# Kernel tuning notes

Measured on AMD Instinct MI355X. Metric: run time of the kernel, lower is better.

The kernel has to match this reference:

```python
import jax, jax.numpy as jnp
import numpy as np

N_QUBITS = 4
N_LAYERS = 2


def _apply_1q_shared(state, gate, wire):
    # state: [N,2,2,2,2] (axis wire+1 = qubit 'wire'), gate: [2,2] complex
    st = jnp.moveaxis(state, wire + 1, -1)
    st = jnp.einsum('ij,nabcj->nabci', gate, st)
    return jnp.moveaxis(st, -1, wire + 1)


def _apply_1q_batched(state, gate, wire):
    # gate: [N,2,2] (per-sample angles)
    st = jnp.moveaxis(state, wire + 1, -1)
    st = jnp.einsum('nij,nabcj->nabci', gate, st)
    return jnp.moveaxis(st, -1, wire + 1)


def _cnot(state, c, t):
    s0 = jnp.take(state, 0, axis=c + 1)
    s1 = jnp.take(state, 1, axis=c + 1)
    t_ax = t if t > c else t + 1  # target axis after removing control axis
    s1 = jnp.flip(s1, axis=t_ax)
    return jnp.stack([s0, s1], axis=c + 1)


def _ry_mat_batched(theta):
    c = jnp.cos(theta / 2).astype(jnp.complex64)
    s = jnp.sin(theta / 2).astype(jnp.complex64)
    return jnp.stack([jnp.stack([c, -s], -1), jnp.stack([s, c], -1)], -2)


def _rx_mat(theta):
    c = jnp.cos(theta / 2).astype(jnp.complex64)
    s = (-1j * jnp.sin(theta / 2)).astype(jnp.complex64)
    return jnp.array(0).astype(jnp.complex64) + jnp.stack([jnp.stack([c, s]), jnp.stack([s, c])])


def _ry_mat(theta):
    c = jnp.cos(theta / 2).astype(jnp.complex64)
    s = jnp.sin(theta / 2).astype(jnp.complex64)
    return jnp.stack([jnp.stack([c, -s]), jnp.stack([s, c])])


def _rz_mat(theta):
    e = jnp.exp(-0.5j * theta.astype(jnp.complex64))
    z = jnp.zeros((), jnp.complex64)
    return jnp.stack([jnp.stack([e, z]), jnp.stack([z, jnp.conj(e)])])


def setup_inputs() -> dict:
    key = jax.random.key(0)
    k1, k2 = jax.random.split(key)
    x = jax.random.normal(k1, (32, 3, 128, 128), dtype=jnp.float32)
    weights = 0.1 * jax.random.normal(k2, (N_LAYERS, N_QUBITS, 3), dtype=jnp.float32)
    return {'x': x, 'weights': weights}


def reference(x, weights):
    B, C, H, W = x.shape
    # 2x2 patches, stride 1, flattened row-major: [N,4]
    patches = jnp.stack(
        [x[:, :, :-1, :-1], x[:, :, :-1, 1:], x[:, :, 1:, :-1], x[:, :, 1:, 1:]],
        axis=-1,
    ).reshape(-1, 4)
    N = patches.shape[0]

    # |0000> state, axis layout [N, q0, q1, q2, q3] (wire 0 most significant)
    state = jnp.zeros((N, 2, 2, 2, 2), jnp.complex64).at[:, 0, 0, 0, 0].set(1.0)

    # RY data encoding (per-patch angles)
    for q in range(N_QUBITS):
        state = _apply_1q_batched(state, _ry_mat_batched(patches[:, q]), q)

    for layer in range(N_LAYERS):
        for q in range(N_QUBITS):
            state = _apply_1q_shared(state, _rx_mat(weights[layer, q, 0]), q)
            state = _apply_1q_shared(state, _ry_mat(weights[layer, q, 1]), q)
            state = _apply_1q_shared(state, _rz_mat(weights[layer, q, 2]), q)
        state = _cnot(state, 0, 1)
        state = _cnot(state, 2, 3)
        state = _cnot(state, 0, 2)
        state = _cnot(state, 1, 3)

    probs = jnp.abs(state) ** 2  # [N,2,2,2,2] real
    ev = probs[:, 0].sum(axis=(1, 2, 3)) - probs[:, 1].sum(axis=(1, 2, 3))  # <Z0>
    return ev.reshape(B, C, H - 1, W - 1).astype(x.dtype)
```

## Files before the change

### kernel.cpp

```cpp
#include <hip/hip_runtime.h>
#include <hip/hip_bf16.h>


__global__ void qconv_setup(const float* __restrict__ wts, float* __restrict__ W) {
    __shared__ float2 U[16][16];
    __shared__ float  A[16][16];
    const int tid = threadIdx.x;

    if (tid < 16) {
        float2 v[16];
        #pragma unroll
        for (int i = 0; i < 16; ++i) v[i] = make_float2(i == tid ? 1.f : 0.f, 0.f);

        #pragma unroll
        for (int layer = 0; layer < 2; ++layer) {
            #pragma unroll
            for (int q = 0; q < 4; ++q) {
                const int p = 3 - q;
                const float thx = wts[(layer * 4 + q) * 3 + 0];
                const float thy = wts[(layer * 4 + q) * 3 + 1];
                const float thz = wts[(layer * 4 + q) * 3 + 2];
                {
                    float c = __cosf(0.5f * thx), s = __sinf(0.5f * thx);
                    #pragma unroll
                    for (int i = 0; i < 16; ++i) if (!((i >> p) & 1)) {
                        const int j = i | (1 << p);
                        float2 a = v[i], b = v[j];
                        v[i] = make_float2(c * a.x + s * b.y, c * a.y - s * b.x);
                        v[j] = make_float2(c * b.x + s * a.y, c * b.y - s * a.x);
                    }
                }
                {
                    float c = __cosf(0.5f * thy), s = __sinf(0.5f * thy);
                    #pragma unroll
                    for (int i = 0; i < 16; ++i) if (!((i >> p) & 1)) {
                        const int j = i | (1 << p);
                        float2 a = v[i], b = v[j];
                        v[i] = make_float2(c * a.x - s * b.x, c * a.y - s * b.y);
                        v[j] = make_float2(s * a.x + c * b.x, s * a.y + c * b.y);
                    }
                }
                {
                    float c = __cosf(0.5f * thz), s = __sinf(0.5f * thz);
                    #pragma unroll
                    for (int i = 0; i < 16; ++i) {
                        float2 a = v[i];
                        if (!((i >> p) & 1)) v[i] = make_float2(c * a.x + s * a.y, c * a.y - s * a.x);
                        else                 v[i] = make_float2(c * a.x - s * a.y, c * a.y + s * a.x);
                    }
                }
            }
            #pragma unroll
            for (int ee = 0; ee < 4; ++ee) {
                const int cc[4] = {0, 2, 0, 1}, tt[4] = {1, 3, 2, 3};
                const int pc = 3 - cc[ee], pt = 3 - tt[ee];
                #pragma unroll
                for (int i = 0; i < 16; ++i) if (((i >> pc) & 1) && !((i >> pt) & 1)) {
                    const int j = i | (1 << pt);
                    float2 t = v[i]; v[i] = v[j]; v[j] = t;
                }
            }
        }
        #pragma unroll
        for (int i = 0; i < 16; ++i) U[tid][i] = v[i];
    }
    __syncthreads();

    {
        const int j = tid >> 4, k = tid & 15;
        float re = 0.f;
        #pragma unroll
        for (int i = 0; i < 16; ++i) {
            const float z = (i & 8) ? -1.f : 1.f;
            float2 a = U[j][i], b = U[k][i];
            re += z * (a.x * b.x + a.y * b.y);
        }
        A[j][k] = re;
    }
    __syncthreads();

    if (tid < 81) {
        const int e = tid;
        const int d0 = e / 27, d1 = (e / 9) % 3, d2 = (e / 3) % 3, d3 = e % 3;
        int mask1 = 0, mask2 = 0;
        if (d0 == 1) mask1 |= 8; else if (d0 == 2) mask2 |= 8;
        if (d1 == 1) mask1 |= 4; else if (d1 == 2) mask2 |= 4;
        if (d2 == 1) mask1 |= 2; else if (d2 == 2) mask2 |= 2;
        if (d3 == 1) mask1 |= 1; else if (d3 == 2) mask2 |= 1;
        float sum = 0.f;
        #pragma unroll
        for (int b = 0; b < 16; ++b) {
            const float sgn = (__popc(b & mask1) & 1) ? -1.f : 1.f;
            sum += sgn * A[b][b ^ mask2];
        }
        W[e] = sum * 0.0625f;
    }
}

__global__ __launch_bounds__(256) void qconv_main(
        const float* __restrict__ x, const float* __restrict__ Wc,
        float* __restrict__ out, int rows) {
    const int g   = blockIdx.x * blockDim.x + threadIdx.x;
    const int row = g >> 5;
    const int l   = g & 31;
    if (row >= rows) return;

    float w[81];
    {
        const float4* W4 = (const float4*)Wc;
        #pragma unroll
        for (int i = 0; i < 20; ++i) {
            float4 v4 = W4[i];
            w[4*i+0] = v4.x; w[4*i+1] = v4.y; w[4*i+2] = v4.z; w[4*i+3] = v4.w;
        }
        w[80] = Wc[80];
    }

    const int img   = row / 127;
    const int h     = row % 127;
    const int col0  = l * 4;
    const int ncols = (l == 31) ? 3 : 4;
    const int base  = img * 16384 + h * 128 + col0;

    float tp[5], bt[5];
    {
        float4 t4 = *(const float4*)(x + base);
        float4 b4 = *(const float4*)(x + base + 128);
        tp[0] = t4.x; tp[1] = t4.y; tp[2] = t4.z; tp[3] = t4.w;
        bt[0] = b4.x; bt[1] = b4.y; bt[2] = b4.z; bt[3] = b4.w;
        tp[4] = 0.f; bt[4] = 0.f;
        if (ncols == 4) { tp[4] = x[base + 4]; bt[4] = x[base + 132]; }
    }

    float ct[5], st[5], cb[5], sb[5];
    #pragma unroll
    for (int j = 0; j < 5; ++j) {
        __sincosf(tp[j], &st[j], &ct[j]);
        __sincosf(bt[j], &sb[j], &cb[j]);
    }

    float ev[4];
    #pragma unroll
    for (int k = 0; k < 4; ++k) {
        const float c0 = ct[k],     s0 = st[k];
        const float c1 = ct[k + 1], s1 = st[k + 1];
        const float c2 = cb[k],     s2 = sb[k];
        const float c3 = cb[k + 1], s3 = sb[k + 1];
        float acc = 0.f;
        #pragma unroll
        for (int e0 = 0; e0 < 3; ++e0) {
            const float u0 = (e0 == 0) ? 1.f : ((e0 == 1) ? c0 : s0);
            float a0 = 0.f;
            #pragma unroll
            for (int e1 = 0; e1 < 3; ++e1) {
                const float u1 = (e1 == 0) ? 1.f : ((e1 == 1) ? c1 : s1);
                float a1 = 0.f;
                #pragma unroll
                for (int e2 = 0; e2 < 3; ++e2) {
                    const float u2 = (e2 == 0) ? 1.f : ((e2 == 1) ? c2 : s2);
                    const int idx = ((e0 * 3 + e1) * 3 + e2) * 3;
                    const float a2 = w[idx] + w[idx + 1] * c3 + w[idx + 2] * s3;
                    a1 += a2 * u2;
                }
                a0 += a1 * u1;
            }
            acc += a0 * u0;
        }
        ev[k] = acc;
    }

    const int obase = row * 127 + col0;
    #pragma unroll
    for (int k = 0; k < 4; ++k) if (k < ncols) out[obase + k] = ev[k];
}

extern "C" void kernel_launch(void* const* d_in, const int* in_sizes, int n_in,
                              void* d_out, int out_size, void* d_ws, size_t ws_size,
                              hipStream_t stream) {
    const float* x   = (const float*)d_in[0];
    const float* wts = (const float*)d_in[1];
    float* out = (float*)d_out;
    float* W   = (float*)d_ws;

    qconv_setup<<<1, 256, 0, stream>>>(wts, W);

    const int rows    = out_size / 127;
    const int threads = rows * 32;
    const int blocks  = (threads + 255) / 256;
    qconv_main<<<blocks, 256, 0, stream>>>(x, W, out, rows);
}
```

Before: 16.88 us.

## Fuse weight-setup into main kernel and process two output rows per thread

Removes the separate single-block setup kernel: every block now recomputes the 81 collapsed circuit coefficients in shared memory before evaluating patches, eliminating a kernel launch and the global round-trip for W. Each thread also handles two adjacent output rows, loading three input rows and reusing the middle row's sin/cos, which cuts input loads and transcendental work per output. The cost is redundant per-block setup work (a 16x16 unitary build plus reductions in every block) and more live registers, which could lower occupancy.

```diff
diff --git a/kernel.cpp b/kernel.cpp
--- a/kernel.cpp
+++ b/kernel.cpp
@@ -2,7 +2,8 @@
 #include <hip/hip_bf16.h>
 
 
-__global__ void qconv_setup(const float* __restrict__ wts, float* __restrict__ W) {
+__device__ __forceinline__ void compute_W_block(const float* __restrict__ wts,
+                                                float* __restrict__ Wsh) {
     __shared__ float2 U[16][16];
     __shared__ float  A[16][16];
     const int tid = threadIdx.x;
@@ -79,73 +80,81 @@
     }
     __syncthreads();
 
-    if (tid < 81) {
-        const int e = tid;
-        const int d0 = e / 27, d1 = (e / 9) % 3, d2 = (e / 3) % 3, d3 = e % 3;
-        int mask1 = 0, mask2 = 0;
-        if (d0 == 1) mask1 |= 8; else if (d0 == 2) mask2 |= 8;
-        if (d1 == 1) mask1 |= 4; else if (d1 == 2) mask2 |= 4;
-        if (d2 == 1) mask1 |= 2; else if (d2 == 2) mask2 |= 2;
-        if (d3 == 1) mask1 |= 1; else if (d3 == 2) mask2 |= 1;
-        float sum = 0.f;
-        #pragma unroll
-        for (int b = 0; b < 16; ++b) {
-            const float sgn = (__popc(b & mask1) & 1) ? -1.f : 1.f;
-            sum += sgn * A[b][b ^ mask2];
-        }
-        W[e] = sum * 0.0625f;
-    }
+    if (tid < 84) {
+        float r = 0.f;
+        if (tid < 81) {
+            const int e = tid;
+            const int d0 = e / 27, d1 = (e / 9) % 3, d2 = (e / 3) % 3, d3 = e % 3;
+            int mask1 = 0, mask2 = 0;
+            if (d0 == 1) mask1 |= 8; else if (d0 == 2) mask2 |= 8;
+            if (d1 == 1) mask1 |= 4; else if (d1 == 2) mask2 |= 4;
+            if (d2 == 1) mask1 |= 2; else if (d2 == 2) mask2 |= 2;
+            if (d3 == 1) mask1 |= 1; else if (d3 == 2) mask2 |= 1;
+            float sum = 0.f;
+            #pragma unroll
+            for (int b = 0; b < 16; ++b) {
+                const float sgn = (__popc(b & mask1) & 1) ? -1.f : 1.f;
+                sum += sgn * A[b][b ^ mask2];
+            }
+            r = sum * 0.0625f;
+        }
+        Wsh[tid] = r;
+    }
+    __syncthreads();
 }
 
-__global__ __launch_bounds__(256) void qconv_main(
-        const float* __restrict__ x, const float* __restrict__ Wc,
-        float* __restrict__ out, int rows) {
-    const int g   = blockIdx.x * blockDim.x + threadIdx.x;
-    const int row = g >> 5;
-    const int l   = g & 31;
-    if (row >= rows) return;
+__global__ __launch_bounds__(256) void qconv_fused(
+        const float* __restrict__ x, const float* __restrict__ wts,
+        float* __restrict__ out) {
+    __shared__ __align__(16) float Wsh[84];
+    compute_W_block(wts, Wsh);
 
     float w[81];
     {
-        const float4* W4 = (const float4*)Wc;
+        const float4* W4 = (const float4*)Wsh;
         #pragma unroll
         for (int i = 0; i < 20; ++i) {
             float4 v4 = W4[i];
             w[4*i+0] = v4.x; w[4*i+1] = v4.y; w[4*i+2] = v4.z; w[4*i+3] = v4.w;
         }
-        w[80] = Wc[80];
-    }
-
-    const int img   = row / 127;
-    const int h     = row % 127;
-    const int col0  = l * 4;
+        w[80] = Wsh[80];
+    }
+
+    const int g    = blockIdx.x * 8 + (threadIdx.x >> 5);
+    const int l    = threadIdx.x & 31;
+    const int img  = g >> 6;
+    const int pair = g & 63;
+    const int h    = pair * 2;
+    const int nr   = (pair == 63) ? 1 : 2;
+    const int col0 = l * 4;
     const int ncols = (l == 31) ? 3 : 4;
-    const int base  = img * 16384 + h * 128 + col0;
-
-    float tp[5], bt[5];
+    const int base = img * 16384 + h * 128 + col0;
+
+    float r0[5], r1[5], r2[5];
     {
-        float4 t4 = *(const float4*)(x + base);
+        float4 a4 = *(const float4*)(x + base);
         float4 b4 = *(const float4*)(x + base + 128);
-        tp[0] = t4.x; tp[1] = t4.y; tp[2] = t4.z; tp[3] = t4.w;
-        bt[0] = b4.x; bt[1] = b4.y; bt[2] = b4.z; bt[3] = b4.w;
-        tp[4] = 0.f; bt[4] = 0.f;
-        if (ncols == 4) { tp[4] = x[base + 4]; bt[4] = x[base + 132]; }
-    }
-
-    float ct[5], st[5], cb[5], sb[5];
+        r0[0]=a4.x; r0[1]=a4.y; r0[2]=a4.z; r0[3]=a4.w;
+        r1[0]=b4.x; r1[1]=b4.y; r1[2]=b4.z; r1[3]=b4.w;
+        r0[4]=0.f; r1[4]=0.f; r2[0]=0.f; r2[1]=0.f; r2[2]=0.f; r2[3]=0.f; r2[4]=0.f;
+        if (ncols == 4) { r0[4] = x[base + 4]; r1[4] = x[base + 132]; }
+        if (nr == 2) {
+            float4 c4 = *(const float4*)(x + base + 256);
+            r2[0]=c4.x; r2[1]=c4.y; r2[2]=c4.z; r2[3]=c4.w;
+            if (ncols == 4) r2[4] = x[base + 260];
+        }
+    }
+
+    float c0a[5], s0a[5], c1a[5], s1a[5], c2a[5], s2a[5];
     #pragma unroll
     for (int j = 0; j < 5; ++j) {
-        __sincosf(tp[j], &st[j], &ct[j]);
-        __sincosf(bt[j], &sb[j], &cb[j]);
-    }
-
-    float ev[4];
-    #pragma unroll
-    for (int k = 0; k < 4; ++k) {
-        const float c0 = ct[k],     s0 = st[k];
-        const float c1 = ct[k + 1], s1 = st[k + 1];
-        const float c2 = cb[k],     s2 = sb[k];
-        const float c3 = cb[k + 1], s3 = sb[k + 1];
+        __sincosf(r0[j], &s0a[j], &c0a[j]);
+        __sincosf(r1[j], &s1a[j], &c1a[j]);
+        __sincosf(r2[j], &s2a[j], &c2a[j]);
+    }
+
+    auto eval = [&](float c0, float s0, float c1, float s1,
+                    float c2, float s2, float c3, float s3) -> float {
         float acc = 0.f;
         #pragma unroll
         for (int e0 = 0; e0 < 3; ++e0) {
@@ -166,12 +175,26 @@
             }
             acc += a0 * u0;
         }
-        ev[k] = acc;
-    }
-
-    const int obase = row * 127 + col0;
+        return acc;
+    };
+
+    float ev0[4], ev1[4];
     #pragma unroll
-    for (int k = 0; k < 4; ++k) if (k < ncols) out[obase + k] = ev[k];
+    for (int k = 0; k < 4; ++k) {
+        ev0[k] = eval(c0a[k], s0a[k], c0a[k+1], s0a[k+1],
+                      c1a[k], s1a[k], c1a[k+1], s1a[k+1]);
+        ev1[k] = eval(c1a[k], s1a[k], c1a[k+1], s1a[k+1],
+                      c2a[k], s2a[k], c2a[k+1], s2a[k+1]);
+    }
+
+    const int ob0 = (img * 127 + h) * 127 + col0;
+    #pragma unroll
+    for (int k = 0; k < 4; ++k) if (k < ncols) out[ob0 + k] = ev0[k];
+    if (nr == 2) {
+        const int ob1 = ob0 + 127;
+        #pragma unroll
+        for (int k = 0; k < 4; ++k) if (k < ncols) out[ob1 + k] = ev1[k];
+    }
 }
 
 extern "C" void kernel_launch(void* const* d_in, const int* in_sizes, int n_in,
@@ -180,12 +203,7 @@
     const float* x   = (const float*)d_in[0];
     const float* wts = (const float*)d_in[1];
     float* out = (float*)d_out;
-    float* W   = (float*)d_ws;
-
-    qconv_setup<<<1, 256, 0, stream>>>(wts, W);
-
-    const int rows    = out_size / 127;
-    const int threads = rows * 32;
-    const int blocks  = (threads + 255) / 256;
-    qconv_main<<<blocks, 256, 0, stream>>>(x, W, out, rows);
+
+    const int blocks = (96 * 64) / 8;
+    qconv_fused<<<blocks, 256, 0, stream>>>(x, wts, out);
 }
```

After: 16.06 us. -4.8%, faster.
